# Kernel tuning notes

Measured on AMD Instinct MI355X. Metric: run time of the kernel, lower is better.

The kernel has to match this reference:

```python
import jax, jax.numpy as jnp
import numpy as np

TAU = 2.0
V_TH = 1.0
ALPHA = 2.0  # ATan surrogate alpha (spikingjelly default)

@jax.custom_vjp
def atan_heaviside(x):
    # Forward: Heaviside spike; backward: ATan surrogate gradient.
    return (x >= 0).astype(x.dtype)

def _atan_fwd(x):
    return atan_heaviside(x), x

def _atan_bwd(x, g):
    sg = (ALPHA / 2.0) / (1.0 + (jnp.pi / 2.0 * ALPHA * x) ** 2)
    return (g * sg,)

atan_heaviside.defvjp(_atan_fwd, _atan_bwd)

def lif_scan(cur):
    # cur: [T, B, F] input currents. LIF: H = V + (X - V)/tau; S = H >= v_th; hard reset V = H*(1-S).
    def step(v, x_t):
        h = v + (x_t - v) / TAU
        s = atan_heaviside(h - V_TH)
        v_new = h * (1.0 - s)
        return v_new, s
    v0 = jnp.zeros(cur.shape[1:], dtype=cur.dtype)
    _, spikes = jax.lax.scan(step, v0, cur)
    return spikes

def setup_inputs() -> dict:
    key = jax.random.key(0)
    k1, k2 = jax.random.split(key)
    T, B, F_in, F_out = 64, 256, 1024, 1024
    x = jax.random.normal(k1, (T, B, F_in), dtype=jnp.float32)
    W = jax.random.normal(k2, (F_out, F_in), dtype=jnp.float32) * (1.0 / np.sqrt(F_in))
    return {"x": x, "W": W}

def reference(x, W):
    # Linear projection over all timesteps, then multi-step LIF recurrence.
    cur = jnp.einsum('tbf,of->tbo', x, W)  # [T, B, F_out]
    return lif_scan(cur)
```

## Files before the change

### kernel.cpp

```cpp
#include <hip/hip_runtime.h>


#define T_DIM 64
#define B_DIM 256
#define F_DIM 1024
#define K_DIM 1024
#define M_DIM 16384
#define COLS  (B_DIM * F_DIM)
#define KP    2048
#define MARGIN 6e-5f
#define LIST_CAP 32768

typedef __attribute__((ext_vector_type(8))) short short8;
typedef __attribute__((ext_vector_type(4))) float floatx4;

#define ASYNC_CP16(gp, lp)                                                     \
    __builtin_amdgcn_global_load_lds(                                          \
        (const __attribute__((address_space(1))) unsigned int*)(gp),           \
        (__attribute__((address_space(3))) unsigned int*)(lp), 16, 0, 0)

#define HARD_SYNC() do {                                                       \
        __builtin_amdgcn_sched_barrier(0);                                     \
        asm volatile("s_waitcnt vmcnt(0) lgkmcnt(0)" ::: "memory");            \
        __syncthreads();                                                       \
        __builtin_amdgcn_sched_barrier(0);                                     \
    } while (0)

__device__ inline unsigned short f32_to_bf16_rne(float f) {
    unsigned int u = __builtin_bit_cast(unsigned int, f);
    unsigned int r = (u + 0x7FFFu + ((u >> 16) & 1u)) >> 16;
    return (unsigned short)r;
}
__device__ inline float bf16_to_f32(unsigned short h) {
    unsigned int u = ((unsigned int)h) << 16;
    return __builtin_bit_cast(float, u);
}

__global__ __launch_bounds__(256) void split_kernel(
    const float* __restrict__ x, const float* __restrict__ Wm,
    unsigned short* __restrict__ A, unsigned short* __restrict__ B,
    unsigned int* __restrict__ counter)
{
    if (blockIdx.x == 0 && threadIdx.x == 0) *counter = 0;
    const int blk = blockIdx.x;
    const float* in;
    unsigned short* dst;
    int g;
    int orow;
    if (blk < 16384) {
        g = blk * 256 + threadIdx.x;
        int e = g * 4;
        int row = e >> 10;
        orow = ((row & 255) << 6) | (row >> 8);
        in = x; dst = A;
    } else {
        g = (blk - 16384) * 256 + threadIdx.x;
        int e = g * 4;
        orow = e >> 10;
        in = Wm; dst = B;
    }
    int k = (g * 4) & 1023;
    float4 v = reinterpret_cast<const float4*>(in)[g];
    ushort4 h, l;
    float f;
    f = v.x; h.x = f32_to_bf16_rne(f); l.x = f32_to_bf16_rne(f - bf16_to_f32(h.x));
    f = v.y; h.y = f32_to_bf16_rne(f); l.y = f32_to_bf16_rne(f - bf16_to_f32(h.y));
    f = v.z; h.z = f32_to_bf16_rne(f); l.z = f32_to_bf16_rne(f - bf16_to_f32(h.z));
    f = v.w; h.w = f32_to_bf16_rne(f); l.w = f32_to_bf16_rne(f - bf16_to_f32(h.w));
    reinterpret_cast<ushort4*>(dst)[(size_t)orow * (KP / 4) + (k >> 2)] = h;
    reinterpret_cast<ushort4*>(dst)[(size_t)orow * (KP / 4) + 256 + (k >> 2)] = l;
}

__global__ __launch_bounds__(512, 2) void gemm_scan_kernel(
    const unsigned short* __restrict__ A,
    const unsigned short* __restrict__ B,
    float* __restrict__ out,
    unsigned int* __restrict__ counter, unsigned int* __restrict__ list)
{
    __shared__ unsigned short Ah0[256 * 32], Al0[256 * 32];
    __shared__ unsigned short Bh0[256 * 32], Bl0[256 * 32];
    __shared__ unsigned short Ah1[256 * 32], Al1[256 * 32];
    __shared__ unsigned short Bh1[256 * 32], Bl1[256 * 32];

    const int tid  = threadIdx.x;
    const int lane = tid & 63;
    const int wv   = tid >> 6;
    const int lid = blockIdx.x;
    const int mt  = ((lid & 7) << 3) | (lid >> 5);
    const int nt  = (lid >> 3) & 3;
    const int m0  = mt * 256;
    const int n0  = nt * 256;
    const int wm  = (wv & 1) * 128;
    const int wn  = (wv >> 1) * 64;

    floatx4 acc[8][4] = {};

    const int srow = tid >> 2;
    const int slin = (tid & 3) * 8;
    const int ssw  = (((tid & 3) ^ ((srow >> 1) & 3)) * 8);
    const int lrow = lane & 15;
    const int q    = lane >> 4;
    const int rsw  = (lrow >> 1) & 3;
    const int sl   = (q ^ rsw) * 8;

    const size_t RKP = (size_t)128 * KP;
    const unsigned short* ga_h = A + (size_t)(m0 + srow) * KP + ssw;
    const unsigned short* ga_l = ga_h + 1024;
    const unsigned short* gb_h = B + (size_t)(n0 + srow) * KP + ssw;
    const unsigned short* gb_l = gb_h + 1024;

    const int ldsA  = srow * 32 + slin;
    const int ldsA2 = (srow + 128) * 32 + slin;

    int aoff[8], boff[4];
#pragma unroll
    for (int i = 0; i < 8; ++i) aoff[i] = (wm + i * 16 + lrow) * 32 + sl;
#pragma unroll
    for (int j = 0; j < 4; ++j) boff[j] = (wn + j * 16 + lrow) * 32 + sl;

#define STAGE(AhB, AlB, BhB, BlB, kk) do {                                     \
        ASYNC_CP16(ga_h + (kk),       &AhB[ldsA]);                             \
        ASYNC_CP16(ga_h + RKP + (kk), &AhB[ldsA2]);                            \
        ASYNC_CP16(ga_l + (kk),       &AlB[ldsA]);                             \
        ASYNC_CP16(ga_l + RKP + (kk), &AlB[ldsA2]);                            \
        ASYNC_CP16(gb_h + (kk),       &BhB[ldsA]);                             \
        ASYNC_CP16(gb_h + RKP + (kk), &BhB[ldsA2]);                            \
        ASYNC_CP16(gb_l + (kk),       &BlB[ldsA]);                             \
        ASYNC_CP16(gb_l + RKP + (kk), &BlB[ldsA2]);                            \
    } while (0)

#define COMPUTE(AhB, AlB, BhB, BlB) do {                                       \
        short8 ah[8], al[8];                                                   \
        _Pragma("unroll")                                                      \
        for (int i = 0; i < 8; ++i) {                                          \
            ah[i] = *reinterpret_cast<const short8*>(&AhB[aoff[i]]);           \
            al[i] = *reinterpret_cast<const short8*>(&AlB[aoff[i]]);           \
        }                                                                      \
        _Pragma("unroll")                                                      \
        for (int jh = 0; jh < 2; ++jh) {                                       \
            short8 bh[2], bl[2];                                               \
            _Pragma("unroll")                                                  \
            for (int j2 = 0; j2 < 2; ++j2) {                                   \
                bh[j2] = *reinterpret_cast<const short8*>(&BhB[boff[jh * 2 + j2]]); \
                bl[j2] = *reinterpret_cast<const short8*>(&BlB[boff[jh * 2 + j2]]); \
            }                                                                  \
            __builtin_amdgcn_s_setprio(1);                                     \
            _Pragma("unroll")                                                  \
            for (int i = 0; i < 8; ++i)                                        \
                _Pragma("unroll")                                              \
                for (int j2 = 0; j2 < 2; ++j2)                                 \
                    acc[i][jh * 2 + j2] = __builtin_amdgcn_mfma_f32_16x16x32_bf16( \
                        ah[i], bh[j2], acc[i][jh * 2 + j2], 0, 0, 0);          \
            _Pragma("unroll")                                                  \
            for (int i = 0; i < 8; ++i)                                        \
                _Pragma("unroll")                                              \
                for (int j2 = 0; j2 < 2; ++j2)                                 \
                    acc[i][jh * 2 + j2] = __builtin_amdgcn_mfma_f32_16x16x32_bf16( \
                        al[i], bh[j2], acc[i][jh * 2 + j2], 0, 0, 0);          \
            _Pragma("unroll")                                                  \
            for (int i = 0; i < 8; ++i)                                        \
                _Pragma("unroll")                                              \
                for (int j2 = 0; j2 < 2; ++j2)                                 \
                    acc[i][jh * 2 + j2] = __builtin_amdgcn_mfma_f32_16x16x32_bf16( \
                        ah[i], bl[j2], acc[i][jh * 2 + j2], 0, 0, 0);          \
            __builtin_amdgcn_s_setprio(0);                                     \
        }                                                                      \
    } while (0)

    STAGE(Ah0, Al0, Bh0, Bl0, 0);
    HARD_SYNC();

#pragma unroll 1
    for (int kt = 0; kt < 32; kt += 2) {
        STAGE(Ah1, Al1, Bh1, Bl1, (kt + 1) * 32);
        COMPUTE(Ah0, Al0, Bh0, Bl0);
        HARD_SYNC();
        if (kt + 2 < 32) STAGE(Ah0, Al0, Bh0, Bl0, (kt + 2) * 32);
        COMPUTE(Ah1, Al1, Bh1, Bl1);
        HARD_SYNC();
    }

#undef STAGE
#undef COMPUTE

    const int col = lane & 15;
    const int b_base = mt * 4 + (wv & 1) * 2;

    unsigned int fmask = 0;
#pragma unroll
    for (int hb = 0; hb < 2; ++hb) {
#pragma unroll
        for (int j = 0; j < 4; ++j) {
            float v = 0.f;
            bool fl = false;
#pragma unroll
            for (int i4 = 0; i4 < 4; ++i4) {
                const int i = hb * 4 + i4;
#pragma unroll
                for (int qq = 0; qq < 4; ++qq) {
                    if (q == qq) {
#pragma unroll
                        for (int r = 0; r < 4; ++r) {
                            float cu = acc[i][j][r];
                            float hm = v + (cu - v) * 0.5f;
                            float d = hm - 1.0f;
                            bool sp = (d >= 0.f);
                            fl |= (fabsf(d) < MARGIN);
                            acc[i][j][r] = sp ? 1.0f : 0.0f;
                            v = sp ? 0.f : hm;
                        }
                    }
                    v = __shfl(v, qq * 16 + col, 64);
                }
            }
            if (fl) fmask |= (1u << (hb * 4 + j));
        }
    }
    fmask |= __shfl_xor(fmask, 16, 64);
    fmask |= __shfl_xor(fmask, 32, 64);

#pragma unroll
    for (int i = 0; i < 8; ++i) {
        float* outp = out + (size_t)(b_base + (i >> 2)) * F_DIM;
        const int tb = (i & 3) * 16 + q * 4;
#pragma unroll
        for (int j = 0; j < 4; ++j)
#pragma unroll
            for (int r = 0; r < 4; ++r)
                outp[(size_t)(tb + r) * COLS + (n0 + wn + j * 16 + col)] = acc[i][j][r];
    }

    if (q == 0 && fmask) {
        for (int hb = 0; hb < 2; ++hb)
            for (int j = 0; j < 4; ++j)
                if (fmask & (1u << (hb * 4 + j))) {
                    unsigned int idx = atomicAdd(counter, 1u);
                    if (idx < LIST_CAP)
                        list[idx] = (unsigned int)(((b_base + hb) << 10) |
                                                   (n0 + wn + j * 16 + col));
                }
    }
}

__global__ __launch_bounds__(256) void fixup_kernel(
    const float* __restrict__ x, const float* __restrict__ W,
    const unsigned int* __restrict__ counter, const unsigned int* __restrict__ list,
    float* __restrict__ out)
{
    __shared__ double curd[T_DIM];
    __shared__ float wrow[K_DIM];
    unsigned int n = *counter;
    if (n > LIST_CAP) n = LIST_CAP;
    const int wv = threadIdx.x >> 6, lane = threadIdx.x & 63;

    for (unsigned int idx = blockIdx.x; idx < n; idx += gridDim.x) {
        const unsigned int c = list[idx];
        const int b = c >> 10, o = c & 1023;
        __syncthreads();
        for (int k = threadIdx.x; k < K_DIM; k += 256) wrow[k] = W[(size_t)o * K_DIM + k];
        __syncthreads();
        for (int it = 0; it < 16; ++it) {
            const int t = it * 4 + wv;
            const float* xp = x + (size_t)t * COLS + (size_t)b * F_DIM + lane * 16;
            double s = 0.0;
#pragma unroll
            for (int qq = 0; qq < 4; ++qq) {
                float4 xv = reinterpret_cast<const float4*>(xp)[qq];
                float4 wq = *reinterpret_cast<const float4*>(&wrow[lane * 16 + qq * 4]);
                s += (double)xv.x * (double)wq.x + (double)xv.y * (double)wq.y +
                     (double)xv.z * (double)wq.z + (double)xv.w * (double)wq.w;
            }
#pragma unroll
            for (int off = 32; off > 0; off >>= 1) s += __shfl_down(s, off, 64);
            if (lane == 0) curd[t] = s;
        }
        __syncthreads();
        if (threadIdx.x == 0) {
            double v = 0.0;
            for (int t = 0; t < T_DIM; ++t) {
                double h = v + (curd[t] - v) * 0.5;
                bool s = (h >= 1.0);
                out[(size_t)t * COLS + c] = s ? 1.0f : 0.0f;
                v = s ? 0.0 : h;
            }
        }
        __syncthreads();
    }
}

#define TILE 64
#define KC 32
#define XS_LD 36
#define SC_LD 65

__global__ __launch_bounds__(256) void lif_fused_kernel(
    const float* __restrict__ x, const float* __restrict__ Wm, float* __restrict__ out)
{
    __shared__ __align__(16) unsigned char smem_raw[TILE * SC_LD * sizeof(double)];
    float* sf = reinterpret_cast<float*>(smem_raw);
    double* sd = reinterpret_cast<double*>(smem_raw);
    float* Xs = sf;
    float* Ws = sf + TILE * XS_LD;

    const int b = blockIdx.y;
    const int o0 = blockIdx.x * TILE;
    const int tid = threadIdx.x;
    const int tx = tid & 15, ty = tid >> 4;

    double acc[4][4];
#pragma unroll
    for (int i = 0; i < 4; ++i)
#pragma unroll
        for (int j = 0; j < 4; ++j) acc[i][j] = 0.0;

    const int r = tid >> 3, c4 = (tid & 7) * 4;
    const float* xbase = x + (size_t)b * F_DIM;

    for (int k0 = 0; k0 < K_DIM; k0 += KC) {
        __syncthreads();
        float4 xv0 = *reinterpret_cast<const float4*>(xbase + (size_t)r * COLS + k0 + c4);
        float4 xv1 = *reinterpret_cast<const float4*>(xbase + (size_t)(r + 32) * COLS + k0 + c4);
        *reinterpret_cast<float4*>(Xs + r * XS_LD + c4) = xv0;
        *reinterpret_cast<float4*>(Xs + (r + 32) * XS_LD + c4) = xv1;
        float4 wv0 = *reinterpret_cast<const float4*>(Wm + (size_t)(o0 + r) * K_DIM + k0 + c4);
        float4 wv1 = *reinterpret_cast<const float4*>(Wm + (size_t)(o0 + r + 32) * K_DIM + k0 + c4);
        *reinterpret_cast<float4*>(Ws + r * XS_LD + c4) = wv0;
        *reinterpret_cast<float4*>(Ws + (r + 32) * XS_LD + c4) = wv1;
        __syncthreads();
#pragma unroll 4
        for (int kk = 0; kk < KC; ++kk) {
            double xa[4], wb[4];
#pragma unroll
            for (int i = 0; i < 4; ++i) xa[i] = (double)Xs[(4 * ty + i) * XS_LD + kk];
#pragma unroll
            for (int j = 0; j < 4; ++j) wb[j] = (double)Ws[(4 * tx + j) * XS_LD + kk];
#pragma unroll
            for (int i = 0; i < 4; ++i)
#pragma unroll
                for (int j = 0; j < 4; ++j) acc[i][j] = fma(xa[i], wb[j], acc[i][j]);
        }
    }
    __syncthreads();
#pragma unroll
    for (int i = 0; i < 4; ++i)
#pragma unroll
        for (int j = 0; j < 4; ++j) sd[(4 * ty + i) * SC_LD + (4 * tx + j)] = acc[i][j];
    __syncthreads();
    if (tid < TILE) {
        double v = 0.0;
        float* outp = out + (size_t)b * F_DIM + o0 + tid;
        for (int t = 0; t < T_DIM; ++t) {
            double cu = sd[t * SC_LD + tid];
            double h = v + (cu - v) * 0.5;
            bool s = (h >= 1.0);
            outp[(size_t)t * COLS] = s ? 1.0f : 0.0f;
            v = s ? 0.0 : h;
        }
    }
}

extern "C" void kernel_launch(void* const* d_in, const int* in_sizes, int n_in,
                              void* d_out, int out_size, void* d_ws, size_t ws_size,
                              hipStream_t stream) {
    const float* x = (const float*)d_in[0];
    const float* Wm = (const float*)d_in[1];
    float* out = (float*)d_out;

    const size_t OFF_A   = 0;
    const size_t OFF_B   = OFF_A + (size_t)M_DIM * KP * 2;
    const size_t OFF_CNT = OFF_B + (size_t)F_DIM * KP * 2;
    const size_t OFF_LST = OFF_CNT + 256;
    const size_t NEEDED  = OFF_LST + (size_t)LIST_CAP * 4;

    if (ws_size < NEEDED) {
        dim3 grid(F_DIM / TILE, B_DIM, 1);
        lif_fused_kernel<<<grid, dim3(256), 0, stream>>>(x, Wm, out);
        return;
    }

    unsigned char* ws = (unsigned char*)d_ws;
    unsigned short* Abuf = (unsigned short*)(ws + OFF_A);
    unsigned short* Bbuf = (unsigned short*)(ws + OFF_B);
    unsigned int* counter = (unsigned int*)(ws + OFF_CNT);
    unsigned int* list = (unsigned int*)(ws + OFF_LST);

    split_kernel<<<dim3(16384 + 1024), dim3(256), 0, stream>>>(x, Wm, Abuf, Bbuf, counter);
    gemm_scan_kernel<<<dim3(256), dim3(512), 0, stream>>>(Abuf, Bbuf, out, counter, list);
    fixup_kernel<<<dim3(512), dim3(256), 0, stream>>>(x, Wm, counter, list, out);
}
```

Measured before the change: 222.5 us.

## Interleave LDS fragment reads with MFMA pairs and split staging across barriers

Restructures the GEMM main loop so each K-tile loads all B fragments once, then reads A fragments two rows at a time, with MFMA pairs between reads and extra workgroup barriers between phases. The async global-to-LDS copies for the next tile are split into A and B halves issued at different points in the tile. The intent is to cut register pressure from holding all A fragments and to interleave LDS reads, global copies and MFMA work so that memory latency overlaps compute better. In exchange it adds four extra __syncthreads per tile, which may cost time if the waves stall on each other.

```diff
diff --git a/kernel.cpp b/kernel.cpp
--- a/kernel.cpp
+++ b/kernel.cpp
@@ -118,70 +118,103 @@
 #pragma unroll
     for (int j = 0; j < 4; ++j) boff[j] = (wn + j * 16 + lrow) * 32 + sl;
 
-#define STAGE(AhB, AlB, BhB, BlB, kk) do {                                     \
-        ASYNC_CP16(ga_h + (kk),       &AhB[ldsA]);                             \
-        ASYNC_CP16(ga_h + RKP + (kk), &AhB[ldsA2]);                            \
-        ASYNC_CP16(ga_l + (kk),       &AlB[ldsA]);                             \
-        ASYNC_CP16(ga_l + RKP + (kk), &AlB[ldsA2]);                            \
-        ASYNC_CP16(gb_h + (kk),       &BhB[ldsA]);                             \
-        ASYNC_CP16(gb_h + RKP + (kk), &BhB[ldsA2]);                            \
-        ASYNC_CP16(gb_l + (kk),       &BlB[ldsA]);                             \
-        ASYNC_CP16(gb_l + RKP + (kk), &BlB[ldsA2]);                            \
-    } while (0)
-
-#define COMPUTE(AhB, AlB, BhB, BlB) do {                                       \
-        short8 ah[8], al[8];                                                   \
-        _Pragma("unroll")                                                      \
-        for (int i = 0; i < 8; ++i) {                                          \
-            ah[i] = *reinterpret_cast<const short8*>(&AhB[aoff[i]]);           \
-            al[i] = *reinterpret_cast<const short8*>(&AlB[aoff[i]]);           \
+#define STAGE_A(AhN, AlN, kk) do {                                             \
+        ASYNC_CP16(ga_h + (kk),       &AhN[ldsA]);                             \
+        ASYNC_CP16(ga_h + RKP + (kk), &AhN[ldsA2]);                            \
+        ASYNC_CP16(ga_l + (kk),       &AlN[ldsA]);                             \
+        ASYNC_CP16(ga_l + RKP + (kk), &AlN[ldsA2]);                            \
+    } while (0)
+
+#define STAGE_B(BhN, BlN, kk) do {                                             \
+        ASYNC_CP16(gb_h + (kk),       &BhN[ldsA]);                             \
+        ASYNC_CP16(gb_h + RKP + (kk), &BhN[ldsA2]);                            \
+        ASYNC_CP16(gb_l + (kk),       &BlN[ldsA]);                             \
+        ASYNC_CP16(gb_l + RKP + (kk), &BlN[ldsA2]);                            \
+    } while (0)
+
+#define READ_B(BhP, BlP) do {                                                  \
+        _Pragma("unroll")                                                      \
+        for (int j = 0; j < 4; ++j) {                                          \
+            bh[j] = *reinterpret_cast<const short8*>(&BhP[boff[j]]);           \
+            bl[j] = *reinterpret_cast<const short8*>(&BlP[boff[j]]);           \
         }                                                                      \
-        _Pragma("unroll")                                                      \
-        for (int jh = 0; jh < 2; ++jh) {                                       \
-            short8 bh[2], bl[2];                                               \
-            _Pragma("unroll")                                                  \
-            for (int j2 = 0; j2 < 2; ++j2) {                                   \
-                bh[j2] = *reinterpret_cast<const short8*>(&BhB[boff[jh * 2 + j2]]); \
-                bl[j2] = *reinterpret_cast<const short8*>(&BlB[boff[jh * 2 + j2]]); \
-            }                                                                  \
-            __builtin_amdgcn_s_setprio(1);                                     \
-            _Pragma("unroll")                                                  \
-            for (int i = 0; i < 8; ++i)                                        \
-                _Pragma("unroll")                                              \
-                for (int j2 = 0; j2 < 2; ++j2)                                 \
-                    acc[i][jh * 2 + j2] = __builtin_amdgcn_mfma_f32_16x16x32_bf16( \
-                        ah[i], bh[j2], acc[i][jh * 2 + j2], 0, 0, 0);          \
-            _Pragma("unroll")                                                  \
-            for (int i = 0; i < 8; ++i)                                        \
-                _Pragma("unroll")                                              \
-                for (int j2 = 0; j2 < 2; ++j2)                                 \
-                    acc[i][jh * 2 + j2] = __builtin_amdgcn_mfma_f32_16x16x32_bf16( \
-                        al[i], bh[j2], acc[i][jh * 2 + j2], 0, 0, 0);          \
-            _Pragma("unroll")                                                  \
-            for (int i = 0; i < 8; ++i)                                        \
-                _Pragma("unroll")                                              \
-                for (int j2 = 0; j2 < 2; ++j2)                                 \
-                    acc[i][jh * 2 + j2] = __builtin_amdgcn_mfma_f32_16x16x32_bf16( \
-                        ah[i], bl[j2], acc[i][jh * 2 + j2], 0, 0, 0);          \
-            __builtin_amdgcn_s_setprio(0);                                     \
-        }                                                                      \
-    } while (0)
-
-    STAGE(Ah0, Al0, Bh0, Bl0, 0);
+    } while (0)
+
+#define READ_A(AhP, AlP, i0) do {                                              \
+        ah0 = *reinterpret_cast<const short8*>(&AhP[aoff[i0]]);                \
+        ah1 = *reinterpret_cast<const short8*>(&AhP[aoff[(i0) + 1]]);          \
+        al0 = *reinterpret_cast<const short8*>(&AlP[aoff[i0]]);                \
+        al1 = *reinterpret_cast<const short8*>(&AlP[aoff[(i0) + 1]]);          \
+    } while (0)
+
+#define MFMA_PAIR(i0) do {                                                     \
+        __builtin_amdgcn_s_setprio(1);                                         \
+        _Pragma("unroll")                                                      \
+        for (int j = 0; j < 4; ++j)                                            \
+            acc[i0][j] = __builtin_amdgcn_mfma_f32_16x16x32_bf16(              \
+                ah0, bh[j], acc[i0][j], 0, 0, 0);                              \
+        _Pragma("unroll")                                                      \
+        for (int j = 0; j < 4; ++j)                                            \
+            acc[(i0) + 1][j] = __builtin_amdgcn_mfma_f32_16x16x32_bf16(        \
+                ah1, bh[j], acc[(i0) + 1][j], 0, 0, 0);                        \
+        _Pragma("unroll")                                                      \
+        for (int j = 0; j < 4; ++j)                                            \
+            acc[i0][j] = __builtin_amdgcn_mfma_f32_16x16x32_bf16(              \
+                al0, bh[j], acc[i0][j], 0, 0, 0);                              \
+        _Pragma("unroll")                                                      \
+        for (int j = 0; j < 4; ++j)                                            \
+            acc[(i0) + 1][j] = __builtin_amdgcn_mfma_f32_16x16x32_bf16(        \
+                al1, bh[j], acc[(i0) + 1][j], 0, 0, 0);                        \
+        _Pragma("unroll")                                                      \
+        for (int j = 0; j < 4; ++j)                                            \
+            acc[i0][j] = __builtin_amdgcn_mfma_f32_16x16x32_bf16(              \
+                ah0, bl[j], acc[i0][j], 0, 0, 0);                              \
+        _Pragma("unroll")                                                      \
+        for (int j = 0; j < 4; ++j)                                            \
+            acc[(i0) + 1][j] = __builtin_amdgcn_mfma_f32_16x16x32_bf16(        \
+                ah1, bl[j], acc[(i0) + 1][j], 0, 0, 0);                        \
+        __builtin_amdgcn_s_setprio(0);                                         \
+    } while (0)
+
+#define TILE_STEP(AhP, AlP, BhP, BlP, AhN, AlN, BhN, BlN, kkn, DO_STAGE) do {  \
+        short8 bh[4], bl[4], ah0, ah1, al0, al1;                               \
+        READ_B(BhP, BlP);                                                      \
+        READ_A(AhP, AlP, 0);                                                   \
+        if (DO_STAGE) STAGE_A(AhN, AlN, kkn);                                  \
+        __syncthreads();                                                       \
+        MFMA_PAIR(0);                                                          \
+        READ_A(AhP, AlP, 2);                                                   \
+        if (DO_STAGE) STAGE_B(BhN, BlN, kkn);                                  \
+        __syncthreads();                                                       \
+        MFMA_PAIR(2);                                                          \
+        READ_A(AhP, AlP, 4);                                                   \
+        __syncthreads();                                                       \
+        MFMA_PAIR(4);                                                          \
+        READ_A(AhP, AlP, 6);                                                   \
+        __syncthreads();                                                       \
+        MFMA_PAIR(6);                                                          \
+        HARD_SYNC();                                                           \
+    } while (0)
+
+    STAGE_A(Ah0, Al0, 0);
+    STAGE_B(Bh0, Bl0, 0);
     HARD_SYNC();
 
 #pragma unroll 1
     for (int kt = 0; kt < 32; kt += 2) {
-        STAGE(Ah1, Al1, Bh1, Bl1, (kt + 1) * 32);
-        COMPUTE(Ah0, Al0, Bh0, Bl0);
-        HARD_SYNC();
-        if (kt + 2 < 32) STAGE(Ah0, Al0, Bh0, Bl0, (kt + 2) * 32);
-        COMPUTE(Ah1, Al1, Bh1, Bl1);
-        HARD_SYNC();
-    }
-
-#undef STAGE
-#undef COMPUTE
+        TILE_STEP(Ah0, Al0, Bh0, Bl0, Ah1, Al1, Bh1, Bl1, (kt + 1) * 32, 1);
+        if (kt + 2 < 32)
+            TILE_STEP(Ah1, Al1, Bh1, Bl1, Ah0, Al0, Bh0, Bl0, (kt + 2) * 32, 1);
+        else
+            TILE_STEP(Ah1, Al1, Bh1, Bl1, Ah0, Al0, Bh0, Bl0, 0, 0);
+    }
+
+#undef TILE_STEP
+#undef MFMA_PAIR
+#undef READ_A
+#undef READ_B
+#undef STAGE_A
+#undef STAGE_B
 
     const int col = lane & 15;
     const int b_base = mt * 4 + (wv & 1) * 2;
```

New measurement: 470.1 us. +111.3%, slower.
